# Kernel optimization log

Hardware: AMD Instinct MI355X
Metric: run time of the kernel (lower is better)

## Reference

```python
import jax, jax.numpy as jnp
import numpy as np

N = 50000      # nodes
E = 800000     # edges (before self-loops)
V = 50000      # vocab
D = 128        # embed_dim
H = 128        # hidden_dim
G = 64         # graphs in batch


def setup_inputs() -> dict:
    key = jax.random.key(0)
    ks = jax.random.split(key, 14)
    x_lex = jax.random.randint(ks[0], (N,), 0, V)
    edge_index = jax.random.randint(ks[1], (2, E), 0, N)
    batch = jnp.sort(jax.random.randint(ks[2], (N,), 0, G))
    s = 1.0 / np.sqrt(D)
    emb = jax.random.normal(ks[3], (V, D), dtype=jnp.float32) * s
    W1 = jax.random.normal(ks[4], (D, H), dtype=jnp.float32) * s
    att_src1 = jax.random.normal(ks[5], (H,), dtype=jnp.float32) * s
    att_dst1 = jax.random.normal(ks[6], (H,), dtype=jnp.float32) * s
    b1 = jnp.zeros((H,), dtype=jnp.float32)
    W2 = jax.random.normal(ks[7], (H, H), dtype=jnp.float32) * s
    att_src2 = jax.random.normal(ks[8], (H,), dtype=jnp.float32) * s
    att_dst2 = jax.random.normal(ks[9], (H,), dtype=jnp.float32) * s
    b2 = jnp.zeros((H,), dtype=jnp.float32)
    Wc = jax.random.normal(ks[10], (H, 1), dtype=jnp.float32) * s
    bc = jnp.zeros((1,), dtype=jnp.float32)
    return dict(x_lex=x_lex, edge_index=edge_index, batch=batch, emb=emb,
                W1=W1, att_src1=att_src1, att_dst1=att_dst1, b1=b1,
                W2=W2, att_src2=att_src2, att_dst2=att_dst2, b2=b2,
                Wc=Wc, bc=bc)


def _gat_conv(x, src, dst, W, a_src, a_dst, b):
    # PyG GATConv, heads=1, self-loops already appended to src/dst.
    h = x @ W                                   # [N, H]
    e = jax.nn.leaky_relu((h @ a_src)[src] + (h @ a_dst)[dst], 0.2)  # [Etot]
    m = jax.ops.segment_max(e, dst, num_segments=N)
    p = jnp.exp(e - m[dst])
    z = jax.ops.segment_sum(p, dst, num_segments=N)
    alpha = p / z[dst]                          # softmax per destination node
    out = jax.ops.segment_sum(alpha[:, None] * h[src], dst, num_segments=N)
    return out + b


def reference(x_lex, edge_index, batch, emb, W1, att_src1, att_dst1, b1,
              W2, att_src2, att_dst2, b2, Wc, bc):
    loops = jnp.arange(N, dtype=edge_index.dtype)
    src = jnp.concatenate([edge_index[0], loops])   # add self-loops (PyG default)
    dst = jnp.concatenate([edge_index[1], loops])
    x = emb[x_lex]                                  # [N, D]
    h = jax.nn.relu(_gat_conv(x, src, dst, W1, att_src1, att_dst1, b1))
    h = jax.nn.relu(_gat_conv(h, src, dst, W2, att_src2, att_dst2, b2))
    sums = jax.ops.segment_sum(h, batch, num_segments=G)           # [G, H]
    cnt = jax.ops.segment_sum(jnp.ones((N,), h.dtype), batch, num_segments=G)
    h_pool = sums / jnp.maximum(cnt, 1.0)[:, None]
    logits = h_pool @ Wc + bc                                       # [G, 1]
    return (logits, h_pool)
```

## Files before the change

kernel.cpp:

```cpp
#include <hip/hip_runtime.h>
#include <hip/hip_bf16.h>


#define THREADS 256
#define PSLICE 16
#define BUK_S 196
#define SORT_BLOCKS 128

typedef __attribute__((ext_vector_type(8))) short short8v;
typedef __attribute__((ext_vector_type(4))) float f32x4;

static __device__ __forceinline__ unsigned short f2bf(float f) {
    unsigned int u = __float_as_uint(f);
    return (unsigned short)((u + 0x7fffu + ((u >> 16) & 1u)) >> 16);
}
static __device__ __forceinline__ float bf2f(unsigned short b) {
    return __uint_as_float(((unsigned int)b) << 16);
}

__global__ __launch_bounds__(THREADS) void k_zero(int* __restrict__ p, int n) {
    int i = blockIdx.x * THREADS + threadIdx.x;
    if (i < n) p[i] = 0;
}

__global__ __launch_bounds__(THREADS) void k_wsplit2(const float* __restrict__ W1,
                                                     const float* __restrict__ W2,
                                                     unsigned short* __restrict__ Wh1,
                                                     unsigned short* __restrict__ Wl1,
                                                     unsigned short* __restrict__ Wh2,
                                                     unsigned short* __restrict__ Wl2) {
    int t = blockIdx.x * THREADS + threadIdx.x;
    const float* W = W1;
    unsigned short* Wh = Wh1;
    unsigned short* Wl = Wl1;
    if (t >= 128 * 128) {
        t -= 128 * 128;
        W = W2; Wh = Wh2; Wl = Wl2;
    }
    int k = t >> 7, n = t & 127;
    float w = W[t];
    unsigned short h = f2bf(w);
    unsigned short lo = f2bf(w - bf2f(h));
    int c = n >> 4, nl = n & 15, tt = k >> 5, kk = k & 31, g = kk >> 3, j = kk & 7;
    int o = (((c * 4 + tt) * 64) + g * 16 + nl) * 8 + j;
    Wh[o] = h;
    Wl[o] = lo;
}

__global__ __launch_bounds__(THREADS) void k_bukhist(const int* __restrict__ dst,
                                                     int* __restrict__ bcount, int E_, int chunk) {
    __shared__ int hist[THREADS];
    hist[threadIdx.x] = 0;
    __syncthreads();
    int e0 = blockIdx.x * chunk;
    int e1 = min(e0 + chunk, E_);
    for (int e = e0 + threadIdx.x; e < e1; e += THREADS)
        atomicAdd(&hist[dst[e] / BUK_S], 1);
    __syncthreads();
    int c = hist[threadIdx.x];
    if (c) atomicAdd(&bcount[threadIdx.x], c);
}

__global__ __launch_bounds__(THREADS) void k_bukscan(const int* __restrict__ bcount,
                                                     int* __restrict__ sbase,
                                                     int* __restrict__ gcur,
                                                     int* __restrict__ cbase,
                                                     int nbuk, int Nn) {
    __shared__ int s[THREADS];
    int tid = threadIdx.x;
    int v = (tid < nbuk) ? bcount[tid] : 0;
    s[tid] = v;
    __syncthreads();
    for (int off = 1; off < THREADS; off <<= 1) {
        int t = (tid >= off) ? s[tid - off] : 0;
        __syncthreads();
        s[tid] += t;
        __syncthreads();
    }
    int excl1 = s[tid] - v;
    if (tid < nbuk) { sbase[tid] = excl1; gcur[tid] = excl1; }
    int n0 = tid * BUK_S;
    int ns = (tid < nbuk) ? min(BUK_S, Nn - n0) : 0;
    int v2 = v + ns;
    __syncthreads();
    s[tid] = v2;
    __syncthreads();
    for (int off = 1; off < THREADS; off <<= 1) {
        int t = (tid >= off) ? s[tid - off] : 0;
        __syncthreads();
        s[tid] += t;
        __syncthreads();
    }
    if (tid < nbuk) cbase[tid] = s[tid] - v2;
}

__global__ __launch_bounds__(THREADS) void k_bukscatter(const int* __restrict__ src,
                                                        const int* __restrict__ dst,
                                                        int* __restrict__ gcur,
                                                        unsigned int* __restrict__ rec,
                                                        int E_, int chunk) {
    __shared__ int hist[THREADS];
    __shared__ int base[THREADS];
    hist[threadIdx.x] = 0;
    __syncthreads();
    int e0 = blockIdx.x * chunk;
    int e1 = min(e0 + chunk, E_);
    for (int e = e0 + threadIdx.x; e < e1; e += THREADS)
        atomicAdd(&hist[dst[e] / BUK_S], 1);
    __syncthreads();
    int c = hist[threadIdx.x];
    if (c) base[threadIdx.x] = atomicAdd(&gcur[threadIdx.x], c);
    hist[threadIdx.x] = 0;
    __syncthreads();
    for (int e = e0 + threadIdx.x; e < e1; e += THREADS) {
        int d = dst[e];
        int b = d / BUK_S;
        int r = atomicAdd(&hist[b], 1);
        rec[base[b] + r] = (unsigned int)src[e] | ((unsigned int)(d - b * BUK_S) << 17);
    }
}

__global__ __launch_bounds__(THREADS) void k_csr(const unsigned int* __restrict__ rec,
                                                 const int* __restrict__ sbase,
                                                 const int* __restrict__ bcount,
                                                 const int* __restrict__ cbase,
                                                 int* __restrict__ rowptr,
                                                 int* __restrict__ esrc,
                                                 int* __restrict__ edst,
                                                 int Nn, int nbuk, int Etot) {
    __shared__ int cnt[THREADS];
    __shared__ int s[THREADS];
    __shared__ int cur[THREADS];
    int b = blockIdx.x;
    int tid = threadIdx.x;
    int n0 = b * BUK_S;
    int ns = min(BUK_S, Nn - n0);
    int cnt_e = bcount[b];
    int rbase = sbase[b];
    int cb = cbase[b];

    cnt[tid] = 0;
    __syncthreads();
    for (int i = tid; i < cnt_e; i += THREADS)
        atomicAdd(&cnt[rec[rbase + i] >> 17], 1);
    __syncthreads();
    int v = (tid < ns) ? cnt[tid] + 1 : 0;
    s[tid] = v;
    __syncthreads();
    for (int off = 1; off < THREADS; off <<= 1) {
        int t = (tid >= off) ? s[tid - off] : 0;
        __syncthreads();
        s[tid] += t;
        __syncthreads();
    }
    int excl = s[tid] - v;
    __syncthreads();
    s[tid] = excl;
    cur[tid] = excl;
    if (tid < ns) rowptr[n0 + tid] = cb + excl;
    if (b == nbuk - 1 && tid == 0) rowptr[Nn] = Etot;
    __syncthreads();
    for (int i = tid; i < cnt_e; i += THREADS) {
        unsigned int r = rec[rbase + i];
        int l = r >> 17;
        int slot = atomicAdd(&cur[l], 1);
        esrc[cb + slot] = (int)(r & 0x1FFFFu);
        edst[cb + slot] = n0 + l;
    }
    __syncthreads();
    if (tid < ns) {
        int slot = s[tid] + cnt[tid];
        esrc[cb + slot] = n0 + tid;
        edst[cb + slot] = n0 + tid;
    }
}

static __device__ __forceinline__ int xsw(int r, int c) {
    return (((r * 16 + (c >> 3)) ^ (r & 7)) << 3) | (c & 7);
}

__global__ __launch_bounds__(THREADS) void k_gemm_mfma(const float* __restrict__ X,
                                                       const int* __restrict__ idx,
                                                       const unsigned short* __restrict__ WBh,
                                                       const unsigned short* __restrict__ WBl,
                                                       const float* __restrict__ a_s,
                                                       const float* __restrict__ a_d,
                                                       unsigned short* __restrict__ outb,
                                                       float* __restrict__ as_,
                                                       float* __restrict__ ad_, int Nrows) {
    __shared__ unsigned short xh[64 * 128];
    __shared__ unsigned short xl[64 * 128];

    {
        int r = threadIdx.x >> 2;
        int c0 = (threadIdx.x & 3) * 32;
        int R = blockIdx.x * 64 + r;
        if (R < Nrows) {
            int g = idx ? idx[R] : R;
            const float4* xrow = (const float4*)(X + (size_t)g * 128);
            #pragma unroll
            for (int i = 0; i < 8; ++i) {
                float4 v = xrow[(c0 >> 2) + i];
                int c = c0 + i * 4;
                ushort4 hh, ll;
                hh.x = f2bf(v.x); ll.x = f2bf(v.x - bf2f(hh.x));
                hh.y = f2bf(v.y); ll.y = f2bf(v.y - bf2f(hh.y));
                hh.z = f2bf(v.z); ll.z = f2bf(v.z - bf2f(hh.z));
                hh.w = f2bf(v.w); ll.w = f2bf(v.w - bf2f(hh.w));
                int o = xsw(r, c);
                *(ushort4*)&xh[o] = hh;
                *(ushort4*)&xl[o] = ll;
            }
        } else {
            #pragma unroll
            for (int i = 0; i < 8; ++i) {
                int o = xsw(r, c0 + i * 4);
                *(ushort4*)&xh[o] = make_ushort4(0, 0, 0, 0);
                *(ushort4*)&xl[o] = make_ushort4(0, 0, 0, 0);
            }
        }
    }
    __syncthreads();

    int wid = threadIdx.x >> 6;
    int lane = threadIdx.x & 63;
    int nl = lane & 15;
    int g = lane >> 4;
    int arow = wid * 16 + nl;

    f32x4 acc[8];
    #pragma unroll
    for (int c = 0; c < 8; ++c) acc[c] = (f32x4){0.f, 0.f, 0.f, 0.f};

    #pragma unroll
    for (int t = 0; t < 4; ++t) {
        int ao = xsw(arow, t * 32 + g * 8);
        short8v ah = *(const short8v*)&xh[ao];
        short8v al = *(const short8v*)&xl[ao];
        #pragma unroll
        for (int c = 0; c < 8; ++c) {
            int bo = (((c * 4 + t) * 64) + lane) * 8;
            short8v bh = *(const short8v*)&WBh[bo];
            short8v bl = *(const short8v*)&WBl[bo];
            acc[c] = __builtin_amdgcn_mfma_f32_16x16x32_bf16(ah, bh, acc[c], 0, 0, 0);
            acc[c] = __builtin_amdgcn_mfma_f32_16x16x32_bf16(ah, bl, acc[c], 0, 0, 0);
            acc[c] = __builtin_amdgcn_mfma_f32_16x16x32_bf16(al, bh, acc[c], 0, 0, 0);
        }
    }

    float asv[8], adv[8];
    #pragma unroll
    for (int c = 0; c < 8; ++c) {
        asv[c] = a_s[c * 16 + nl];
        adv[c] = a_d[c * 16 + nl];
    }
    int Rb = blockIdx.x * 64 + wid * 16 + g * 4;
    #pragma unroll
    for (int r = 0; r < 4; ++r) {
        int R = Rb + r;
        bool ok = (R < Nrows);
        float ps = 0.f, pd = 0.f;
        #pragma unroll
        for (int c = 0; c < 8; ++c) {
            float v = acc[c][r];
            if (ok) outb[(size_t)R * 128 + c * 16 + nl] = f2bf(v);
            ps = fmaf(v, asv[c], ps);
            pd = fmaf(v, adv[c], pd);
        }
        #pragma unroll
        for (int o = 8; o; o >>= 1) {
            ps += __shfl_xor(ps, o);
            pd += __shfl_xor(pd, o);
        }
        if (ok && nl == 0) {
            as_[R] = ps;
            ad_[R] = pd;
        }
    }
}

__global__ __launch_bounds__(THREADS) void k_edgep(const float* __restrict__ as_,
                                                   const float* __restrict__ ad_,
                                                   const int* __restrict__ esrc,
                                                   const int* __restrict__ edst,
                                                   float* __restrict__ pbuf, int Etot, int Epad) {
    int k = blockIdx.x * THREADS + threadIdx.x;
    if (k >= Epad) return;
    if (k < Etot) {
        float e = as_[esrc[k]] + ad_[edst[k]];
        e = (e > 0.f) ? e : 0.2f * e;
        pbuf[k] = __expf(e);
    } else {
        pbuf[k] = 0.f;
    }
}

__global__ __launch_bounds__(THREADS) void k_agg(const unsigned short* __restrict__ hb,
                                                 const float* __restrict__ pbuf,
                                                 const int* __restrict__ rowptr,
                                                 const int* __restrict__ esrc,
                                                 const float* __restrict__ bias,
                                                 float* __restrict__ out, int Nn, int Etot) {
    int d = blockIdx.x * 4 + (threadIdx.x >> 6);
    int lane = threadIdx.x & 63;
    int half = lane >> 5;
    int j = lane & 31;
    if (d >= Nn) return;
    int beg = rowptr[d], end = rowptr[d + 1];
    float z = 0.f, a0 = 0.f, a1 = 0.f, a2 = 0.f, a3 = 0.f;
    for (int k0 = beg; k0 < end; k0 += 16) {
        int sv[8];
        float pv[8];
        #pragma unroll
        for (int i = 0; i < 8; ++i) {
            int kk = k0 + 2 * i + half;
            bool ok = (kk < end);
            sv[i] = esrc[min(kk, Etot - 1)];
            pv[i] = ok ? pbuf[kk] : 0.f;
        }
        uint2 hv[8];
        #pragma unroll
        for (int i = 0; i < 8; ++i)
            hv[i] = *(const uint2*)&hb[((size_t)sv[i] << 7) + j * 4];
        #pragma unroll
        for (int i = 0; i < 8; ++i) {
            float p = pv[i];
            z += p;
            a0 += p * __uint_as_float(hv[i].x << 16);
            a1 += p * __uint_as_float(hv[i].x & 0xffff0000u);
            a2 += p * __uint_as_float(hv[i].y << 16);
            a3 += p * __uint_as_float(hv[i].y & 0xffff0000u);
        }
    }
    z  += __shfl_xor(z, 32);
    a0 += __shfl_xor(a0, 32);
    a1 += __shfl_xor(a1, 32);
    a2 += __shfl_xor(a2, 32);
    a3 += __shfl_xor(a3, 32);
    if (half == 0) {
        float inv = 1.f / z;
        float4 o;
        o.x = fmaxf(a0 * inv + bias[j * 4 + 0], 0.f);
        o.y = fmaxf(a1 * inv + bias[j * 4 + 1], 0.f);
        o.z = fmaxf(a2 * inv + bias[j * 4 + 2], 0.f);
        o.w = fmaxf(a3 * inv + bias[j * 4 + 3], 0.f);
        *(float4*)&out[(size_t)d * 128 + j * 4] = o;
    }
}

__global__ __launch_bounds__(THREADS) void k_pool_partial(const float* __restrict__ x,
                                                          const int* __restrict__ batch,
                                                          float* __restrict__ part, int Nn) {
    int g = blockIdx.x;
    int s = blockIdx.y;
    int a = 0, b = Nn;
    while (a < b) { int mid = (a + b) >> 1; if (batch[mid] < g) a = mid + 1; else b = mid; }
    int lo = a;
    b = Nn;
    while (a < b) { int mid = (a + b) >> 1; if (batch[mid] < g + 1) a = mid + 1; else b = mid; }
    int hi = a;

    int j = threadIdx.x & 127;
    int half = threadIdx.x >> 7;
    float acc = 0.f;
    for (int n = lo + s * 2 + half; n < hi; n += 2 * PSLICE) acc += x[(size_t)n * 128 + j];
    __shared__ float sred[THREADS];
    sred[threadIdx.x] = acc;
    __syncthreads();
    if (half == 0) part[((size_t)g * PSLICE + s) * 128 + j] = sred[j] + sred[128 + j];
}

__global__ __launch_bounds__(128) void k_pool_final(const float* __restrict__ part,
                                                    const int* __restrict__ batch,
                                                    const float* __restrict__ Wc,
                                                    const float* __restrict__ bc,
                                                    float* __restrict__ out, int Nn, int Gn) {
    int g = blockIdx.x;
    int j = threadIdx.x;
    int a = 0, b = Nn;
    while (a < b) { int mid = (a + b) >> 1; if (batch[mid] < g) a = mid + 1; else b = mid; }
    int lo = a;
    b = Nn;
    while (a < b) { int mid = (a + b) >> 1; if (batch[mid] < g + 1) a = mid + 1; else b = mid; }
    int cnt = a - lo;

    float s = 0.f;
    #pragma unroll
    for (int t = 0; t < PSLICE; ++t) s += part[((size_t)g * PSLICE + t) * 128 + j];
    float mean = s / fmaxf((float)cnt, 1.f);
    out[Gn + (size_t)g * 128 + j] = mean;

    __shared__ float sred[128];
    sred[j] = mean * Wc[j];
    __syncthreads();
    for (int off = 64; off >= 1; off >>= 1) {
        if (j < off) sred[j] += sred[j + off];
        __syncthreads();
    }
    if (j == 0) out[g] = sred[0] + bc[0];
}

static inline size_t align256(size_t x) { return (x + 255) & ~(size_t)255; }

extern "C" void kernel_launch(void* const* d_in, const int* in_sizes, int n_in,
                              void* d_out, int out_size, void* d_ws, size_t ws_size,
                              hipStream_t stream) {
    const int* x_lex = (const int*)d_in[0];
    const int* eidx  = (const int*)d_in[1];
    const int* batch = (const int*)d_in[2];
    const float* emb = (const float*)d_in[3];
    const float* W1  = (const float*)d_in[4];
    const float* a_s1 = (const float*)d_in[5];
    const float* a_d1 = (const float*)d_in[6];
    const float* b1  = (const float*)d_in[7];
    const float* W2  = (const float*)d_in[8];
    const float* a_s2 = (const float*)d_in[9];
    const float* a_d2 = (const float*)d_in[10];
    const float* b2  = (const float*)d_in[11];
    const float* Wc  = (const float*)d_in[12];
    const float* bc  = (const float*)d_in[13];

    const int N = in_sizes[0];
    const int E = in_sizes[1] / 2;
    const int G = out_size / 129;
    const int Etot = E + N;
    const int Epad = Etot + 16;
    const int* esrc_in = eidx;
    const int* edst_in = eidx + E;
    const int NBUK = (N + BUK_S - 1) / BUK_S;

    char* p = (char*)d_ws;
    unsigned short* hb = (unsigned short*)p;  p += align256((size_t)N * 128 * 2);
    float* obuf = (float*)p;            p += align256((size_t)N * 128 * 4);
    float* as_  = (float*)p;            p += align256((size_t)N * 4);
    float* ad_  = (float*)p;            p += align256((size_t)N * 4);
    int* bcount = (int*)p;              p += align256((size_t)NBUK * 4);
    int* sbase  = (int*)p;              p += align256((size_t)NBUK * 4);
    int* gcur   = (int*)p;              p += align256((size_t)NBUK * 4);
    int* cbase  = (int*)p;              p += align256((size_t)NBUK * 4);
    int* rowptr = (int*)p;              p += align256((size_t)(N + 1) * 4);
    unsigned int* rec = (unsigned int*)p; p += align256((size_t)Epad * 4);
    int* esrc   = (int*)p;              p += align256((size_t)Etot * 4);
    int* edst   = (int*)p;              p += align256((size_t)Etot * 4);
    float* part = (float*)p;            p += align256((size_t)G * PSLICE * 128 * 4);
    unsigned short* WBh1 = (unsigned short*)p; p += align256((size_t)128 * 128 * 2);
    unsigned short* WBl1 = (unsigned short*)p; p += align256((size_t)128 * 128 * 2);
    unsigned short* WBh2 = (unsigned short*)p; p += align256((size_t)128 * 128 * 2);
    unsigned short* WBl2 = (unsigned short*)p; p += align256((size_t)128 * 128 * 2);
    float* pbuf = (float*)rec;

    const int chunk = (E + SORT_BLOCKS - 1) / SORT_BLOCKS;

    k_wsplit2<<<128, THREADS, 0, stream>>>(W1, W2, WBh1, WBl1, WBh2, WBl2);

    k_zero<<<1, THREADS, 0, stream>>>(bcount, NBUK);
    k_bukhist<<<SORT_BLOCKS, THREADS, 0, stream>>>(edst_in, bcount, E, chunk);
    k_bukscan<<<1, THREADS, 0, stream>>>(bcount, sbase, gcur, cbase, NBUK, N);
    k_bukscatter<<<SORT_BLOCKS, THREADS, 0, stream>>>(esrc_in, edst_in, gcur, rec, E, chunk);
    k_csr<<<NBUK, THREADS, 0, stream>>>(rec, sbase, bcount, cbase, rowptr, esrc, edst, N, NBUK, Etot);

    const int gemm_grid = (N + 63) / 64;
    const int agg_grid = (N + 3) / 4;
    const int edge_grid = (Epad + THREADS - 1) / THREADS;

    k_gemm_mfma<<<gemm_grid, THREADS, 0, stream>>>(emb, x_lex, WBh1, WBl1, a_s1, a_d1, hb, as_, ad_, N);
    k_edgep<<<edge_grid, THREADS, 0, stream>>>(as_, ad_, esrc, edst, pbuf, Etot, Epad);
    k_agg<<<agg_grid, THREADS, 0, stream>>>(hb, pbuf, rowptr, esrc, b1, obuf, N, Etot);

    k_gemm_mfma<<<gemm_grid, THREADS, 0, stream>>>(obuf, nullptr, WBh2, WBl2, a_s2, a_d2, hb, as_, ad_, N);
    k_edgep<<<edge_grid, THREADS, 0, stream>>>(as_, ad_, esrc, edst, pbuf, Etot, Epad);
    k_agg<<<agg_grid, THREADS, 0, stream>>>(hb, pbuf, rowptr, esrc, b2, obuf, N, Etot);

    k_pool_partial<<<dim3(G, PSLICE), THREADS, 0, stream>>>(obuf, batch, part, N);
    k_pool_final<<<G, 128, 0, stream>>>(part, batch, Wc, bc, (float*)d_out, N, G);
}
```

Baseline: 198.2 us.

## Fuse edge attention exponent into aggregation kernel and fold bucket-count zeroing

Removes the separate per-edge kernel that computed exp(leaky_relu(as[src]+ad[dst])) into a global buffer. Each aggregation wavefront now loads 64 edge sources at a time, computes their weights itself, and stages index/weight pairs in shared memory before the gather loop. This drops two launches and the write and reread of the per-edge weight array for both layers. The bucket-count zeroing also moves into the weight-split kernel, removing one more launch. In exchange the aggregation kernel carries extra per-chunk latency and uses shared memory, and the within-wave LDS handoff relies on lockstep execution with no barrier.

```diff
diff --git a/kernel.cpp b/kernel.cpp
--- a/kernel.cpp
+++ b/kernel.cpp
@@ -16,11 +16,6 @@
 }
 static __device__ __forceinline__ float bf2f(unsigned short b) {
     return __uint_as_float(((unsigned int)b) << 16);
-}
-
-__global__ __launch_bounds__(THREADS) void k_zero(int* __restrict__ p, int n) {
-    int i = blockIdx.x * THREADS + threadIdx.x;
-    if (i < n) p[i] = 0;
 }
 
 __global__ __launch_bounds__(THREADS) void k_wsplit2(const float* __restrict__ W1,
@@ -28,7 +23,9 @@
                                                      unsigned short* __restrict__ Wh1,
                                                      unsigned short* __restrict__ Wl1,
                                                      unsigned short* __restrict__ Wh2,
-                                                     unsigned short* __restrict__ Wl2) {
+                                                     unsigned short* __restrict__ Wl2,
+                                                     int* __restrict__ bcount, int nbuk) {
+    if (blockIdx.x == 0 && threadIdx.x < nbuk) bcount[threadIdx.x] = 0;
     int t = blockIdx.x * THREADS + threadIdx.x;
     const float* W = W1;
     unsigned short* Wh = Wh1;
@@ -279,57 +276,54 @@
     }
 }
 
-__global__ __launch_bounds__(THREADS) void k_edgep(const float* __restrict__ as_,
-                                                   const float* __restrict__ ad_,
-                                                   const int* __restrict__ esrc,
-                                                   const int* __restrict__ edst,
-                                                   float* __restrict__ pbuf, int Etot, int Epad) {
-    int k = blockIdx.x * THREADS + threadIdx.x;
-    if (k >= Epad) return;
-    if (k < Etot) {
-        float e = as_[esrc[k]] + ad_[edst[k]];
-        e = (e > 0.f) ? e : 0.2f * e;
-        pbuf[k] = __expf(e);
-    } else {
-        pbuf[k] = 0.f;
-    }
-}
-
 __global__ __launch_bounds__(THREADS) void k_agg(const unsigned short* __restrict__ hb,
-                                                 const float* __restrict__ pbuf,
+                                                 const float* __restrict__ as_,
+                                                 const float* __restrict__ ad_,
                                                  const int* __restrict__ rowptr,
                                                  const int* __restrict__ esrc,
                                                  const float* __restrict__ bias,
-                                                 float* __restrict__ out, int Nn, int Etot) {
-    int d = blockIdx.x * 4 + (threadIdx.x >> 6);
+                                                 float* __restrict__ out, int Nn) {
+    __shared__ int2 ep[4][64];
+    int w = threadIdx.x >> 6;
     int lane = threadIdx.x & 63;
     int half = lane >> 5;
     int j = lane & 31;
+    int d = blockIdx.x * 4 + w;
     if (d >= Nn) return;
     int beg = rowptr[d], end = rowptr[d + 1];
+    float adv = ad_[d];
     float z = 0.f, a0 = 0.f, a1 = 0.f, a2 = 0.f, a3 = 0.f;
-    for (int k0 = beg; k0 < end; k0 += 16) {
-        int sv[8];
-        float pv[8];
-        #pragma unroll
-        for (int i = 0; i < 8; ++i) {
-            int kk = k0 + 2 * i + half;
-            bool ok = (kk < end);
-            sv[i] = esrc[min(kk, Etot - 1)];
-            pv[i] = ok ? pbuf[kk] : 0.f;
-        }
-        uint2 hv[8];
-        #pragma unroll
-        for (int i = 0; i < 8; ++i)
-            hv[i] = *(const uint2*)&hb[((size_t)sv[i] << 7) + j * 4];
-        #pragma unroll
-        for (int i = 0; i < 8; ++i) {
-            float p = pv[i];
-            z += p;
-            a0 += p * __uint_as_float(hv[i].x << 16);
-            a1 += p * __uint_as_float(hv[i].x & 0xffff0000u);
-            a2 += p * __uint_as_float(hv[i].y << 16);
-            a3 += p * __uint_as_float(hv[i].y & 0xffff0000u);
+    for (int c0 = beg; c0 < end; c0 += 64) {
+        int kk = c0 + lane;
+        bool ok = (kk < end);
+        int sl = esrc[ok ? kk : beg];
+        float pv = 0.f;
+        if (ok) {
+            float e = as_[sl] + adv;
+            e = (e > 0.f) ? e : 0.2f * e;
+            pv = __expf(e);
+        }
+        ep[w][lane] = make_int2(sl, __float_as_int(pv));
+        int cn = end - c0;
+        if (cn > 64) cn = 64;
+        for (int k0 = 0; k0 < cn; k0 += 16) {
+            int2 ev[8];
+            #pragma unroll
+            for (int i = 0; i < 8; ++i)
+                ev[i] = ep[w][(k0 + 2 * i + half) & 63];
+            uint2 hv[8];
+            #pragma unroll
+            for (int i = 0; i < 8; ++i)
+                hv[i] = *(const uint2*)&hb[((size_t)ev[i].x << 7) + j * 4];
+            #pragma unroll
+            for (int i = 0; i < 8; ++i) {
+                float p = __int_as_float(ev[i].y);
+                z += p;
+                a0 += p * __uint_as_float(hv[i].x << 16);
+                a1 += p * __uint_as_float(hv[i].x & 0xffff0000u);
+                a2 += p * __uint_as_float(hv[i].y << 16);
+                a3 += p * __uint_as_float(hv[i].y & 0xffff0000u);
+            }
         }
     }
     z  += __shfl_xor(z, 32);
@@ -424,7 +418,6 @@
     const int E = in_sizes[1] / 2;
     const int G = out_size / 129;
     const int Etot = E + N;
-    const int Epad = Etot + 16;
     const int* esrc_in = eidx;
     const int* edst_in = eidx + E;
     const int NBUK = (N + BUK_S - 1) / BUK_S;
@@ -439,7 +432,7 @@
     int* gcur   = (int*)p;              p += align256((size_t)NBUK * 4);
     int* cbase  = (int*)p;              p += align256((size_t)NBUK * 4);
     int* rowptr = (int*)p;              p += align256((size_t)(N + 1) * 4);
-    unsigned int* rec = (unsigned int*)p; p += align256((size_t)Epad * 4);
+    unsigned int* rec = (unsigned int*)p; p += align256((size_t)Etot * 4);
     int* esrc   = (int*)p;              p += align256((size_t)Etot * 4);
     int* edst   = (int*)p;              p += align256((size_t)Etot * 4);
     float* part = (float*)p;            p += align256((size_t)G * PSLICE * 128 * 4);
@@ -447,13 +440,11 @@
     unsigned short* WBl1 = (unsigned short*)p; p += align256((size_t)128 * 128 * 2);
     unsigned short* WBh2 = (unsigned short*)p; p += align256((size_t)128 * 128 * 2);
     unsigned short* WBl2 = (unsigned short*)p; p += align256((size_t)128 * 128 * 2);
-    float* pbuf = (float*)rec;
 
     const int chunk = (E + SORT_BLOCKS - 1) / SORT_BLOCKS;
 
-    k_wsplit2<<<128, THREADS, 0, stream>>>(W1, W2, WBh1, WBl1, WBh2, WBl2);
-
-    k_zero<<<1, THREADS, 0, stream>>>(bcount, NBUK);
+    k_wsplit2<<<128, THREADS, 0, stream>>>(W1, W2, WBh1, WBl1, WBh2, WBl2, bcount, NBUK);
+
     k_bukhist<<<SORT_BLOCKS, THREADS, 0, stream>>>(edst_in, bcount, E, chunk);
     k_bukscan<<<1, THREADS, 0, stream>>>(bcount, sbase, gcur, cbase, NBUK, N);
     k_bukscatter<<<SORT_BLOCKS, THREADS, 0, stream>>>(esrc_in, edst_in, gcur, rec, E, chunk);
@@ -461,15 +452,12 @@
 
     const int gemm_grid = (N + 63) / 64;
     const int agg_grid = (N + 3) / 4;
-    const int edge_grid = (Epad + THREADS - 1) / THREADS;
 
     k_gemm_mfma<<<gemm_grid, THREADS, 0, stream>>>(emb, x_lex, WBh1, WBl1, a_s1, a_d1, hb, as_, ad_, N);
-    k_edgep<<<edge_grid, THREADS, 0, stream>>>(as_, ad_, esrc, edst, pbuf, Etot, Epad);
-    k_agg<<<agg_grid, THREADS, 0, stream>>>(hb, pbuf, rowptr, esrc, b1, obuf, N, Etot);
+    k_agg<<<agg_grid, THREADS, 0, stream>>>(hb, as_, ad_, rowptr, esrc, b1, obuf, N);
 
     k_gemm_mfma<<<gemm_grid, THREADS, 0, stream>>>(obuf, nullptr, WBh2, WBl2, a_s2, a_d2, hb, as_, ad_, N);
-    k_edgep<<<edge_grid, THREADS, 0, stream>>>(as_, ad_, esrc, edst, pbuf, Etot, Epad);
-    k_agg<<<agg_grid, THREADS, 0, stream>>>(hb, pbuf, rowptr, esrc, b2, obuf, N, Etot);
+    k_agg<<<agg_grid, THREADS, 0, stream>>>(hb, as_, ad_, rowptr, esrc, b2, obuf, N);
 
     k_pool_partial<<<dim3(G, PSLICE), THREADS, 0, stream>>>(obuf, batch, part, N);
     k_pool_final<<<G, 128, 0, stream>>>(part, batch, Wc, bc, (float*)d_out, N, G);
```

Result: faster. 180.5 us (-9.0%).
